# Kernel optimization log

Measured on AMD Instinct MI355X. Metric: run time of the kernel, lower is better.

Reference implementation:

```python
import jax, jax.numpy as jnp
import numpy as np

MARGIN = 0.1
N = 16384


def setup_inputs() -> dict:
    key = jax.random.key(0)
    k1, k2 = jax.random.split(key)
    pred = jax.random.normal(k1, (N,), dtype=jnp.float32)
    target = jax.random.uniform(k2, (N,), dtype=jnp.float32)
    return {"pred": pred, "target": target}


def reference(pred, target):
    # mask[i, j] = target[j] < target[i]  (the Python loop's Tj per row i)
    mask = target[None, :] < target[:, None]            # [N, N] bool
    # hinge[i, j] = max(0, margin - (pred[i] - pred[j]))
    hinge = jnp.maximum(0.0, MARGIN - (pred[:, None] - pred[None, :]))
    row_sum = jnp.sum(jnp.where(mask, hinge, 0.0), axis=1)   # [N]
    cnt = jnp.sum(mask, axis=1)                               # [N] int
    # rows with no j such that target[j] < target[i] are skipped (continue)
    per_row = jnp.where(cnt > 0, row_sum / jnp.maximum(cnt, 1).astype(pred.dtype), 0.0)
    return jnp.sum(per_row) / pred.shape[0]
```

## Files before the change

kernel.cpp:

```cpp
#include <hip/hip_runtime.h>


constexpr float MARGIN = 0.1f;
constexpr int T   = 256;
constexpr int R1  = 16;
constexpr int R2  = 8;

__global__ __launch_bounds__(T) void rank_scatter(const float* __restrict__ pred,
                                                  const float* __restrict__ target,
                                                  float* __restrict__ p_sorted,
                                                  int* __restrict__ K_sorted,
                                                  unsigned int* __restrict__ tie_ctr,
                                                  int n) {
    const int base = blockIdx.x * R1;

    float ti[R1];
    #pragma unroll
    for (int r = 0; r < R1; ++r) ti[r] = target[base + r];

    unsigned int cnt[R1];
    #pragma unroll
    for (int r = 0; r < R1; ++r) cnt[r] = 0u;

    const float4* __restrict__ t4 = (const float4*)target;
    const int n4 = n >> 2;

    for (int j = (int)threadIdx.x; j < n4; j += T) {
        const float4 tj = t4[j];
        #pragma unroll
        for (int r = 0; r < R1; ++r) {
            const float tir = ti[r];
            cnt[r] += (tj.x < tir) ? 1u : 0u;
            cnt[r] += (tj.y < tir) ? 1u : 0u;
            cnt[r] += (tj.z < tir) ? 1u : 0u;
            cnt[r] += (tj.w < tir) ? 1u : 0u;
        }
    }

    __shared__ unsigned int lc[T / 64][R1];
    const int lane = threadIdx.x & 63;
    const int wv   = threadIdx.x >> 6;

    #pragma unroll
    for (int r = 0; r < R1; ++r) {
        unsigned int c = cnt[r];
        #pragma unroll
        for (int off = 32; off > 0; off >>= 1) c += __shfl_down(c, off, 64);
        if (lane == 0) lc[wv][r] = c;
    }
    __syncthreads();

    if ((int)threadIdx.x < R1) {
        const int r = threadIdx.x;
        const unsigned int strict = lc[0][r] + lc[1][r] + lc[2][r] + lc[3][r];
        const int slot = (int)strict + (int)atomicAdd(&tie_ctr[strict], 1u);
        p_sorted[slot] = pred[base + r];
        K_sorted[slot] = (int)strict;
    }
}

__global__ __launch_bounds__(T) void hinge_sorted(const float* __restrict__ p_sorted,
                                                  const int* __restrict__ K_sorted,
                                                  float* __restrict__ partials,
                                                  int n) {
    const int base = blockIdx.x * R2;

    float c[R2];
    int   K[R2];
    #pragma unroll
    for (int r = 0; r < R2; ++r) {
        K[r] = K_sorted[base + r];
        c[r] = MARGIN - p_sorted[base + r];
    }
    const int Kmin = K[0];
    const int Kmax = K[R2 - 1];

    float sum[R2];
    #pragma unroll
    for (int r = 0; r < R2; ++r) sum[r] = 0.f;

    const float4* __restrict__ p4 = (const float4*)p_sorted;
    const int n4m = Kmin >> 2;
    for (int j = (int)threadIdx.x; j < n4m; j += T) {
        const float4 p = p4[j];
        #pragma unroll
        for (int r = 0; r < R2; ++r) {
            const float cr = c[r];
            sum[r] += fmaxf(0.f, cr + p.x);
            sum[r] += fmaxf(0.f, cr + p.y);
            sum[r] += fmaxf(0.f, cr + p.z);
            sum[r] += fmaxf(0.f, cr + p.w);
        }
    }

    for (int j = (n4m << 2) + (int)threadIdx.x; j < Kmax; j += T) {
        const float pj = p_sorted[j];
        #pragma unroll
        for (int r = 0; r < R2; ++r) {
            sum[r] += (j < K[r]) ? fmaxf(0.f, c[r] + pj) : 0.f;
        }
    }

    __shared__ float ls[T / 64][R2];
    __shared__ float row_val[R2];
    const int lane = threadIdx.x & 63;
    const int wv   = threadIdx.x >> 6;

    #pragma unroll
    for (int r = 0; r < R2; ++r) {
        float s = sum[r];
        #pragma unroll
        for (int off = 32; off > 0; off >>= 1) s += __shfl_down(s, off, 64);
        if (lane == 0) ls[wv][r] = s;
    }
    __syncthreads();

    if ((int)threadIdx.x < R2) {
        const int r = threadIdx.x;
        const float s = ls[0][r] + ls[1][r] + ls[2][r] + ls[3][r];
        row_val[r] = (K[r] > 0) ? (s / (float)K[r]) : 0.f;
    }
    __syncthreads();

    if (threadIdx.x == 0) {
        float local = 0.f;
        #pragma unroll
        for (int r = 0; r < R2; ++r) local += row_val[r];
        partials[blockIdx.x] = local;
    }
}

__global__ __launch_bounds__(T) void final_reduce(const float* __restrict__ partials,
                                                  float* __restrict__ out,
                                                  int nblk, float inv_n) {
    const float4* __restrict__ pr4 = (const float4*)partials;
    const int n4 = nblk >> 2;
    float s = 0.f;
    for (int j = (int)threadIdx.x; j < n4; j += T) {
        const float4 v = pr4[j];
        s += v.x + v.y + v.z + v.w;
    }
    #pragma unroll
    for (int off = 32; off > 0; off >>= 1) s += __shfl_down(s, off, 64);

    __shared__ float sd[T / 64];
    const int lane = threadIdx.x & 63;
    const int wv   = threadIdx.x >> 6;
    if (lane == 0) sd[wv] = s;
    __syncthreads();
    if (threadIdx.x == 0) {
        out[0] = (sd[0] + sd[1] + sd[2] + sd[3]) * inv_n;
    }
}

extern "C" void kernel_launch(void* const* d_in, const int* in_sizes, int n_in,
                              void* d_out, int out_size, void* d_ws, size_t ws_size,
                              hipStream_t stream) {
    const float* pred   = (const float*)d_in[0];
    const float* target = (const float*)d_in[1];
    const int n = in_sizes[0];
    const int nblk2 = n / R2;

    float*        p_sorted = (float*)d_ws;
    int*          K_sorted = (int*)((char*)d_ws + (size_t)n * 4);
    unsigned int* tie_ctr  = (unsigned int*)((char*)d_ws + (size_t)n * 8);
    float*        partials = (float*)((char*)d_ws + (size_t)n * 12);

    hipMemsetAsync(tie_ctr, 0, (size_t)n * 4, stream);

    rank_scatter<<<n / R1, T, 0, stream>>>(pred, target, p_sorted, K_sorted, tie_ctr, n);
    hinge_sorted<<<nblk2, T, 0, stream>>>(p_sorted, K_sorted, partials, n);
    final_reduce<<<1, T, 0, stream>>>(partials, (float*)d_out, nblk2, 1.0f / (float)n);
}
```

Baseline: 92.47 us.

## Pair low and high rank groups per block and fuse final reduction via atomics

The hinge kernel now launches a fixed 1024 blocks, and each block handles two row groups, one from the start of the sorted order and one from the end. Because work per row grows with rank, pairing them evens out the load across blocks. The separate final-reduce kernel is removed: blocks atomically add their totals into an accumulator, and the last block to finish writes the scaled result. This drops one kernel launch and the tail imbalance, at the cost of a nondeterministic float summation order and atomic contention on a single address.

```diff
diff --git a/kernel.cpp b/kernel.cpp
--- a/kernel.cpp
+++ b/kernel.cpp
@@ -5,6 +5,7 @@
 constexpr int T   = 256;
 constexpr int R1  = 16;
 constexpr int R2  = 8;
+constexpr int NB2 = 1024;
 
 __global__ __launch_bounds__(T) void rank_scatter(const float* __restrict__ pred,
                                                   const float* __restrict__ target,
@@ -61,95 +62,89 @@
 
 __global__ __launch_bounds__(T) void hinge_sorted(const float* __restrict__ p_sorted,
                                                   const int* __restrict__ K_sorted,
-                                                  float* __restrict__ partials,
-                                                  int n) {
-    const int base = blockIdx.x * R2;
+                                                  float* __restrict__ acc,
+                                                  unsigned int* __restrict__ done,
+                                                  float* __restrict__ out,
+                                                  int n, float inv_n) {
+    const int lane = threadIdx.x & 63;
+    const int wv   = threadIdx.x >> 6;
 
-    float c[R2];
-    int   K[R2];
+    __shared__ float ls[T / 64][R2];
+    __shared__ float row_val[R2];
+
+    float block_total = 0.f;
+
     #pragma unroll
-    for (int r = 0; r < R2; ++r) {
-        K[r] = K_sorted[base + r];
-        c[r] = MARGIN - p_sorted[base + r];
-    }
-    const int Kmin = K[0];
-    const int Kmax = K[R2 - 1];
+    for (int g = 0; g < 2; ++g) {
+        const int base = (g == 0) ? (int)blockIdx.x * R2
+                                  : n - R2 - (int)blockIdx.x * R2;
 
-    float sum[R2];
-    #pragma unroll
-    for (int r = 0; r < R2; ++r) sum[r] = 0.f;
-
-    const float4* __restrict__ p4 = (const float4*)p_sorted;
-    const int n4m = Kmin >> 2;
-    for (int j = (int)threadIdx.x; j < n4m; j += T) {
-        const float4 p = p4[j];
+        float c[R2];
+        int   K[R2];
         #pragma unroll
         for (int r = 0; r < R2; ++r) {
-            const float cr = c[r];
-            sum[r] += fmaxf(0.f, cr + p.x);
-            sum[r] += fmaxf(0.f, cr + p.y);
-            sum[r] += fmaxf(0.f, cr + p.z);
-            sum[r] += fmaxf(0.f, cr + p.w);
+            K[r] = K_sorted[base + r];
+            c[r] = MARGIN - p_sorted[base + r];
+        }
+        const int Kmin = K[0];
+        const int Kmax = K[R2 - 1];
+
+        float sum[R2];
+        #pragma unroll
+        for (int r = 0; r < R2; ++r) sum[r] = 0.f;
+
+        const float4* __restrict__ p4 = (const float4*)p_sorted;
+        const int n4m = Kmin >> 2;
+        for (int j = (int)threadIdx.x; j < n4m; j += T) {
+            const float4 p = p4[j];
+            #pragma unroll
+            for (int r = 0; r < R2; ++r) {
+                const float cr = c[r];
+                sum[r] += fmaxf(0.f, cr + p.x);
+                sum[r] += fmaxf(0.f, cr + p.y);
+                sum[r] += fmaxf(0.f, cr + p.z);
+                sum[r] += fmaxf(0.f, cr + p.w);
+            }
+        }
+        for (int j = (n4m << 2) + (int)threadIdx.x; j < Kmax; j += T) {
+            const float pj = p_sorted[j];
+            #pragma unroll
+            for (int r = 0; r < R2; ++r) {
+                sum[r] += (j < K[r]) ? fmaxf(0.f, c[r] + pj) : 0.f;
+            }
+        }
+
+        __syncthreads();
+        #pragma unroll
+        for (int r = 0; r < R2; ++r) {
+            float s = sum[r];
+            #pragma unroll
+            for (int off = 32; off > 0; off >>= 1) s += __shfl_down(s, off, 64);
+            if (lane == 0) ls[wv][r] = s;
+        }
+        __syncthreads();
+
+        if ((int)threadIdx.x < R2) {
+            const int r = threadIdx.x;
+            const float s = ls[0][r] + ls[1][r] + ls[2][r] + ls[3][r];
+            row_val[r] = (K[r] > 0) ? (s / (float)K[r]) : 0.f;
+        }
+        __syncthreads();
+
+        if (threadIdx.x == 0) {
+            #pragma unroll
+            for (int r = 0; r < R2; ++r) block_total += row_val[r];
         }
     }
 
-    for (int j = (n4m << 2) + (int)threadIdx.x; j < Kmax; j += T) {
-        const float pj = p_sorted[j];
-        #pragma unroll
-        for (int r = 0; r < R2; ++r) {
-            sum[r] += (j < K[r]) ? fmaxf(0.f, c[r] + pj) : 0.f;
+    if (threadIdx.x == 0) {
+        atomicAdd(acc, block_total);
+        __threadfence();
+        const unsigned int old = atomicAdd(done, 1u);
+        if (old == (unsigned int)(gridDim.x - 1)) {
+            const float total = atomicAdd(acc, 0.0f);
+            out[0] = total * inv_n;
         }
-    }
-
-    __shared__ float ls[T / 64][R2];
-    __shared__ float row_val[R2];
-    const int lane = threadIdx.x & 63;
-    const int wv   = threadIdx.x >> 6;
-
-    #pragma unroll
-    for (int r = 0; r < R2; ++r) {
-        float s = sum[r];
-        #pragma unroll
-        for (int off = 32; off > 0; off >>= 1) s += __shfl_down(s, off, 64);
-        if (lane == 0) ls[wv][r] = s;
-    }
-    __syncthreads();
-
-    if ((int)threadIdx.x < R2) {
-        const int r = threadIdx.x;
-        const float s = ls[0][r] + ls[1][r] + ls[2][r] + ls[3][r];
-        row_val[r] = (K[r] > 0) ? (s / (float)K[r]) : 0.f;
-    }
-    __syncthreads();
-
-    if (threadIdx.x == 0) {
-        float local = 0.f;
-        #pragma unroll
-        for (int r = 0; r < R2; ++r) local += row_val[r];
-        partials[blockIdx.x] = local;
-    }
-}
-
-__global__ __launch_bounds__(T) void final_reduce(const float* __restrict__ partials,
-                                                  float* __restrict__ out,
-                                                  int nblk, float inv_n) {
-    const float4* __restrict__ pr4 = (const float4*)partials;
-    const int n4 = nblk >> 2;
-    float s = 0.f;
-    for (int j = (int)threadIdx.x; j < n4; j += T) {
-        const float4 v = pr4[j];
-        s += v.x + v.y + v.z + v.w;
-    }
-    #pragma unroll
-    for (int off = 32; off > 0; off >>= 1) s += __shfl_down(s, off, 64);
-
-    __shared__ float sd[T / 64];
-    const int lane = threadIdx.x & 63;
-    const int wv   = threadIdx.x >> 6;
-    if (lane == 0) sd[wv] = s;
-    __syncthreads();
-    if (threadIdx.x == 0) {
-        out[0] = (sd[0] + sd[1] + sd[2] + sd[3]) * inv_n;
     }
 }
 
@@ -159,16 +154,16 @@
     const float* pred   = (const float*)d_in[0];
     const float* target = (const float*)d_in[1];
     const int n = in_sizes[0];
-    const int nblk2 = n / R2;
 
     float*        p_sorted = (float*)d_ws;
     int*          K_sorted = (int*)((char*)d_ws + (size_t)n * 4);
     unsigned int* tie_ctr  = (unsigned int*)((char*)d_ws + (size_t)n * 8);
-    float*        partials = (float*)((char*)d_ws + (size_t)n * 12);
+    float*        acc      = (float*)((char*)d_ws + (size_t)n * 12);
+    unsigned int* done     = (unsigned int*)((char*)d_ws + (size_t)n * 12 + 4);
 
-    hipMemsetAsync(tie_ctr, 0, (size_t)n * 4, stream);
+    hipMemsetAsync(tie_ctr, 0, (size_t)n * 4 + 8, stream);
 
     rank_scatter<<<n / R1, T, 0, stream>>>(pred, target, p_sorted, K_sorted, tie_ctr, n);
-    hinge_sorted<<<nblk2, T, 0, stream>>>(p_sorted, K_sorted, partials, n);
-    final_reduce<<<1, T, 0, stream>>>(partials, (float*)d_out, nblk2, 1.0f / (float)n);
+    hinge_sorted<<<NB2, T, 0, stream>>>(p_sorted, K_sorted, acc, done,
+                                        (float*)d_out, n, 1.0f / (float)n);
 }
```

New measurement: 116.0 us. 1.25x slower.
